# Kernel tuning notes

Hardware: AMD Instinct MI355X
Metric: run time of the kernel (lower is better)

The kernel has to match this reference:

```python
import jax, jax.numpy as jnp
import numpy as np

SIGMA = 0.5          # cone height of the distance field
B, NV, NF, MAXC = 32, 6890, 13776, 8
NC = NF * MAXC       # padded number of collision pair slots


def setup_inputs() -> dict:
    key = jax.random.key(0)
    ks = jax.random.split(key, 8)
    return {
        "pose": jax.random.normal(ks[0], (B, 72), jnp.float32),
        "joints": jax.random.normal(ks[1], (B, 24, 3), jnp.float32),
        "points": jax.random.normal(ks[2], (B, 118, 3), jnp.float32),
        "keypoints": jax.random.normal(ks[3], (B, 118, 3), jnp.float32),
        "vertices": jax.random.normal(ks[4], (B, NV, 3), jnp.float32),
        "weight": jnp.ones((1,), jnp.float32),
        "faces": jax.random.randint(ks[5], (NF, 3), 0, NV, dtype=jnp.int32),
        "collision_idxs": jax.random.randint(ks[6], (B, NC, 2), 0, NF, dtype=jnp.int32),
    }


def _cone_point2plane(cone_tris, query_tris):
    """Conic distance-field penetration (point2plane), vectorized over pairs.
    cone_tris/query_tris: [B, C, 3 verts, 3 xyz]. Returns [B, C]."""
    c = cone_tris.mean(axis=-2)                              # centroid [B,C,3]
    e1 = cone_tris[..., 1, :] - cone_tris[..., 0, :]
    e2 = cone_tris[..., 2, :] - cone_tris[..., 0, :]
    n = jnp.cross(e1, e2)
    n = n / (jnp.linalg.norm(n, axis=-1, keepdims=True) + 1e-8)
    d = query_tris - c[..., None, :]                         # [B,C,3,3]
    h = jnp.einsum('bcvk,bck->bcv', d, n)                    # signed plane dist
    r = jnp.linalg.norm(d, axis=-1)                          # dist to centroid
    phi = jnp.maximum(SIGMA - r, 0.0)                        # linear cone field
    pen = jnp.where(h < 0, phi * h * h, 0.0)                 # penetrating verts only
    return pen.sum(axis=-1)


def reference(pose, joints, points, keypoints, vertices, weight, faces, collision_idxs):
    # polygons = verts.view(-1,3)[faces_idx]  ->  per-batch face gather
    tris = jnp.take(vertices, faces, axis=1)                 # [B,NF,3,3]
    recv_idx = collision_idxs[..., 0]
    intr_idx = collision_idxs[..., 1]
    valid = recv_idx >= 0                                    # -1 padding slots

    def gather(idx):
        idx = jnp.maximum(idx, 0)[:, :, None, None]
        return jnp.take_along_axis(tris, idx, axis=1)        # [B,NC,3,3]

    recv = gather(recv_idx)
    intr = gather(intr_idx)
    # symmetric penetration: intruder verts in receiver's field and vice versa
    pen = _cone_point2plane(recv, intr) + _cone_point2plane(intr, recv)
    loss = jnp.where(valid, pen, 0.0).sum() / B
    return loss * weight[0]
```

## Files before the change

### kernel.cpp

```cpp
#include <hip/hip_runtime.h>

#define SIGMA 0.5f
#define BB 32
#define NVV 6890
#define NFF 13776
#define MAXC 8
#define NCC (NFF * MAXC)

#define SLOTS 8
#define PAIRS_PER_SLOT (NCC / SLOTS)
#define QHALF (PAIRS_PER_SLOT / 4)
#define THREADS 1024
#define NBLOCK (BB * SLOTS)

typedef int       v4i __attribute__((ext_vector_type(4)));
typedef _Float16  h4  __attribute__((ext_vector_type(4)));

__device__ __forceinline__ float3 loadv3(const float* __restrict__ p) {
    return make_float3(p[0], p[1], p[2]);
}

__device__ __forceinline__ float fsqrt(float x) { return __builtin_amdgcn_sqrtf(x); }
__device__ __forceinline__ float frcp(float x)  { return __builtin_amdgcn_rcpf(x); }

__device__ __forceinline__ float coneSide(float cx, float cy, float cz,
                                          float nx, float ny, float nz,
                                          float3 q0, float3 q1, float3 q2) {
    float pen = 0.0f;
#pragma unroll
    for (int v = 0; v < 3; ++v) {
        float3 q = (v == 0) ? q0 : ((v == 1) ? q1 : q2);
        float dx = q.x - cx, dy = q.y - cy, dz = q.z - cz;
        float h  = dx * nx + dy * ny + dz * nz;
        float r2 = dx * dx + dy * dy + dz * dz;
        float r  = fsqrt(r2);
        float phi = fmaxf(SIGMA - r, 0.0f);
        float hm  = fminf(h, 0.0f);
        pen = fmaf(phi * hm, hm, pen);
    }
    return pen;
}

__device__ __forceinline__ float triPairPen(float3 A0, float3 A1, float3 A2,
                                            float3 B0, float3 B1, float3 B2) {
    const float third = 1.0f / 3.0f;
    float cax = (A0.x + A1.x + A2.x) * third;
    float cay = (A0.y + A1.y + A2.y) * third;
    float caz = (A0.z + A1.z + A2.z) * third;
    float cbx = (B0.x + B1.x + B2.x) * third;
    float cby = (B0.y + B1.y + B2.y) * third;
    float cbz = (B0.z + B1.z + B2.z) * third;
    float e1x = A1.x - A0.x, e1y = A1.y - A0.y, e1z = A1.z - A0.z;
    float e2x = A2.x - A0.x, e2y = A2.y - A0.y, e2z = A2.z - A0.z;
    float nax = e1y * e2z - e1z * e2y;
    float nay = e1z * e2x - e1x * e2z;
    float naz = e1x * e2y - e1y * e2x;
    float inva = frcp(fsqrt(nax * nax + nay * nay + naz * naz) + 1e-8f);
    nax *= inva; nay *= inva; naz *= inva;
    float f1x = B1.x - B0.x, f1y = B1.y - B0.y, f1z = B1.z - B0.z;
    float f2x = B2.x - B0.x, f2y = B2.y - B0.y, f2z = B2.z - B0.z;
    float nbx = f1y * f2z - f1z * f2y;
    float nby = f1z * f2x - f1x * f2z;
    float nbz = f1x * f2y - f1y * f2x;
    float invb = frcp(fsqrt(nbx * nbx + nby * nby + nbz * nbz) + 1e-8f);
    nbx *= invb; nby *= invb; nbz *= invb;

    return coneSide(cax, cay, caz, nax, nay, naz, B0, B1, B2)
         + coneSide(cbx, cby, cbz, nbx, nby, nbz, A0, A1, A2);
}

__device__ __forceinline__ float3 ldsVertB(const h4* __restrict__ sv, unsigned int boff) {
    h4 h = *(const h4*)((const char*)sv + boff);
    return make_float3((float)h.x, (float)h.y, (float)h.z);
}

__device__ __forceinline__ float pairPen(const h4* __restrict__ sv,
                                         const unsigned int*   __restrict__ f01,
                                         const unsigned short* __restrict__ f2,
                                         int r, int it) {
    const int rr = r  < 0 ? 0 : r;
    const int g  = it < 0 ? 0 : it;
    unsigned int wa  = f01[rr];
    unsigned int wb  = f01[g];
    unsigned int oa2 = f2[rr];
    unsigned int ob2 = f2[g];
    float3 A0 = ldsVertB(sv, wa & 0xFFFFu);
    float3 A1 = ldsVertB(sv, wa >> 16);
    float3 A2 = ldsVertB(sv, oa2);
    float3 B0 = ldsVertB(sv, wb & 0xFFFFu);
    float3 B1 = ldsVertB(sv, wb >> 16);
    float3 B2 = ldsVertB(sv, ob2);
    float pen = triPairPen(A0, A1, A2, B0, B1, B2);
    return r < 0 ? 0.0f : pen;
}

__global__ __launch_bounds__(THREADS) void fused_kernel(
    const float* __restrict__ vertices,
    const int*   __restrict__ faces,
    const int*   __restrict__ cidx,
    float*       __restrict__ partials)
{
    __shared__ h4             s_v[NVV];
    __shared__ unsigned int   s_f01[NFF];
    __shared__ unsigned short s_f2[NFF];
    __shared__ float          s_red[16];

    const int b   = blockIdx.x;
    const int sl  = blockIdx.y;
    const int tid = threadIdx.x;

    const float* vb = vertices + (size_t)b * (NVV * 3);
    for (int v = tid; v < NVV; v += THREADS) {
        const float* p = vb + 3 * v;
        h4 h;
        h.x = (_Float16)p[0];
        h.y = (_Float16)p[1];
        h.z = (_Float16)p[2];
        h.w = (_Float16)0.0f;
        s_v[v] = h;
    }

    for (int f = tid; f < NFF; f += THREADS) {
        int i0 = faces[3 * f + 0];
        int i1 = faces[3 * f + 1];
        int i2 = faces[3 * f + 2];
        s_f01[f] = (unsigned int)(i0 << 3) | ((unsigned int)(i1 << 3) << 16);
        s_f2[f]  = (unsigned short)(i2 << 3);
    }
    __syncthreads();

    float pen = 0.0f;
    const v4i* c4 = (const v4i*)(cidx + ((size_t)b * NCC + (size_t)sl * PAIRS_PER_SLOT) * 2);
    for (int q = tid; q < QHALF; q += THREADS) {
        v4i pA = __builtin_nontemporal_load(c4 + q);
        v4i pB = __builtin_nontemporal_load(c4 + q + QHALF);
        float p0 = pairPen(s_v, s_f01, s_f2, pA.x, pA.y);
        float p1 = pairPen(s_v, s_f01, s_f2, pA.z, pA.w);
        float p2 = pairPen(s_v, s_f01, s_f2, pB.x, pB.y);
        float p3 = pairPen(s_v, s_f01, s_f2, pB.z, pB.w);
        pen += (p0 + p1) + (p2 + p3);
    }

#pragma unroll
    for (int off = 32; off > 0; off >>= 1)
        pen += __shfl_down(pen, off, 64);
    const int lane = tid & 63;
    const int wv   = tid >> 6;
    if (lane == 0) s_red[wv] = pen;
    __syncthreads();
    if (tid == 0) {
        float t = 0.0f;
#pragma unroll
        for (int w = 0; w < 16; ++w) t += s_red[w];
        partials[b * SLOTS + sl] = t;
    }
}

__global__ __launch_bounds__(256) void fin2_kernel(
    const float* __restrict__ partials,
    const float* __restrict__ weight,
    float*       __restrict__ out)
{
    float s = partials[threadIdx.x];
#pragma unroll
    for (int off = 32; off > 0; off >>= 1)
        s += __shfl_down(s, off, 64);
    __shared__ float smem[4];
    const int lane = threadIdx.x & 63;
    const int wv   = threadIdx.x >> 6;
    if (lane == 0) smem[wv] = s;
    __syncthreads();
    if (threadIdx.x == 0)
        out[0] = (smem[0] + smem[1] + smem[2] + smem[3]) * weight[0] * (1.0f / (float)BB);
}

__global__ void init_kernel(float* __restrict__ accum) { accum[0] = 0.0f; }

__global__ __launch_bounds__(256) void pen_direct(
    const float* __restrict__ vertices, const int* __restrict__ faces,
    const int2* __restrict__ cidx, float* __restrict__ accum)
{
    const int i = blockIdx.x * blockDim.x + threadIdx.x;
    float pen = 0.0f;
    if (i < BB * NCC) {
        const int b = i / NCC;
        const int2 pr = cidx[i];
        if (pr.x >= 0) {
            const int f0 = pr.x;
            const int f1 = pr.y < 0 ? 0 : pr.y;
            const float* vb = vertices + (size_t)b * (NVV * 3);
            float3 a0 = loadv3(vb + (size_t)faces[f0*3+0] * 3);
            float3 a1 = loadv3(vb + (size_t)faces[f0*3+1] * 3);
            float3 a2 = loadv3(vb + (size_t)faces[f0*3+2] * 3);
            float3 b0 = loadv3(vb + (size_t)faces[f1*3+0] * 3);
            float3 b1 = loadv3(vb + (size_t)faces[f1*3+1] * 3);
            float3 b2 = loadv3(vb + (size_t)faces[f1*3+2] * 3);
            pen = triPairPen(a0, a1, a2, b0, b1, b2);
        }
    }
#pragma unroll
    for (int off = 32; off > 0; off >>= 1)
        pen += __shfl_down(pen, off, 64);
    __shared__ float smem[4];
    const int lane = threadIdx.x & 63;
    const int wv   = threadIdx.x >> 6;
    if (lane == 0) smem[wv] = pen;
    __syncthreads();
    if (threadIdx.x == 0)
        atomicAdd(accum, smem[0] + smem[1] + smem[2] + smem[3]);
}

__global__ void fin_kernel(const float* __restrict__ accum,
                           const float* __restrict__ weight,
                           float* __restrict__ out)
{
    out[0] = accum[0] * weight[0] * (1.0f / (float)BB);
}

extern "C" void kernel_launch(void* const* d_in, const int* in_sizes, int n_in,
                              void* d_out, int out_size, void* d_ws, size_t ws_size,
                              hipStream_t stream) {
    const float* vertices = (const float*)d_in[4];
    const float* weight   = (const float*)d_in[5];
    const int*   faces    = (const int*)d_in[6];
    const int*   cidx     = (const int*)d_in[7];
    float* out = (float*)d_out;

    if (ws_size >= NBLOCK * sizeof(float)) {
        float* partials = (float*)d_ws;
        fused_kernel<<<dim3(BB, SLOTS), dim3(THREADS), 0, stream>>>(
            vertices, faces, cidx, partials);
        fin2_kernel<<<dim3(1), dim3(256), 0, stream>>>(partials, weight, out);
    } else {
        float* accum = (float*)d_ws;
        const int totalPairs = BB * NCC;
        init_kernel<<<dim3(1), dim3(1), 0, stream>>>(accum);
        pen_direct<<<dim3((totalPairs + 255) / 256), dim3(256), 0, stream>>>(
            vertices, faces, (const int2*)cidx, accum);
        fin_kernel<<<dim3(1), dim3(1), 0, stream>>>(accum, weight, out);
    }
}
```

Measured before the change: 111.8 us.

## Move packed face table to global memory and double slot count

Face index packing moves out of the main kernel into a separate pack kernel that writes a uint2 table to workspace. The fused kernel then reads face offsets from global (L2-cached) memory instead of rebuilding them in LDS for every block. This removes a redundant per-block face pass and shrinks LDS to just the fp16 vertex cache, so more blocks can fit per CU. Slots go from 8 to 16, which doubles the grid to 512 blocks. The cost is that every vertex lookup now follows a global-memory gather, and vertices are still re-staged into LDS by twice as many blocks.

Measured after the change: 135.6 us. 21.3% more time.

```diff
diff --git a/kernel.cpp b/kernel.cpp
--- a/kernel.cpp
+++ b/kernel.cpp
@@ -7,11 +7,14 @@
 #define MAXC 8
 #define NCC (NFF * MAXC)
 
-#define SLOTS 8
+#define SLOTS 16
 #define PAIRS_PER_SLOT (NCC / SLOTS)
-#define QHALF (PAIRS_PER_SLOT / 4)
+#define QUADS (PAIRS_PER_SLOT / 2)
 #define THREADS 1024
 #define NBLOCK (BB * SLOTS)
+
+#define FTAB_BYTES ((size_t)NFF * 8)
+#define WS_NEED (FTAB_BYTES + (size_t)NBLOCK * 4 + 64)
 
 typedef int       v4i __attribute__((ext_vector_type(4)));
 typedef _Float16  h4  __attribute__((ext_vector_type(4)));
@@ -74,36 +77,43 @@
     return make_float3((float)h.x, (float)h.y, (float)h.z);
 }
 
-__device__ __forceinline__ float pairPen(const h4* __restrict__ sv,
-                                         const unsigned int*   __restrict__ f01,
-                                         const unsigned short* __restrict__ f2,
+__device__ __forceinline__ float pairPen(const h4*   __restrict__ sv,
+                                         const uint2* __restrict__ ftab,
                                          int r, int it) {
     const int rr = r  < 0 ? 0 : r;
     const int g  = it < 0 ? 0 : it;
-    unsigned int wa  = f01[rr];
-    unsigned int wb  = f01[g];
-    unsigned int oa2 = f2[rr];
-    unsigned int ob2 = f2[g];
-    float3 A0 = ldsVertB(sv, wa & 0xFFFFu);
-    float3 A1 = ldsVertB(sv, wa >> 16);
-    float3 A2 = ldsVertB(sv, oa2);
-    float3 B0 = ldsVertB(sv, wb & 0xFFFFu);
-    float3 B1 = ldsVertB(sv, wb >> 16);
-    float3 B2 = ldsVertB(sv, ob2);
+    uint2 fa = ftab[rr];
+    uint2 fb = ftab[g];
+    float3 A0 = ldsVertB(sv, fa.x & 0xFFFFu);
+    float3 A1 = ldsVertB(sv, fa.x >> 16);
+    float3 A2 = ldsVertB(sv, fa.y);
+    float3 B0 = ldsVertB(sv, fb.x & 0xFFFFu);
+    float3 B1 = ldsVertB(sv, fb.x >> 16);
+    float3 B2 = ldsVertB(sv, fb.y);
     float pen = triPairPen(A0, A1, A2, B0, B1, B2);
     return r < 0 ? 0.0f : pen;
 }
 
-__global__ __launch_bounds__(THREADS) void fused_kernel(
+__global__ __launch_bounds__(256) void pack_kernel(
+    const int* __restrict__ faces,
+    uint2*     __restrict__ ftab)
+{
+    const int f = blockIdx.x * 256 + threadIdx.x;
+    if (f >= NFF) return;
+    const unsigned int o0 = (unsigned int)(faces[3 * f + 0] << 3);
+    const unsigned int o1 = (unsigned int)(faces[3 * f + 1] << 3);
+    const unsigned int o2 = (unsigned int)(faces[3 * f + 2] << 3);
+    ftab[f] = make_uint2(o0 | (o1 << 16), o2);
+}
+
+__global__ __launch_bounds__(THREADS, 8) void fused_kernel(
     const float* __restrict__ vertices,
-    const int*   __restrict__ faces,
+    const uint2* __restrict__ ftab,
     const int*   __restrict__ cidx,
     float*       __restrict__ partials)
 {
-    __shared__ h4             s_v[NVV];
-    __shared__ unsigned int   s_f01[NFF];
-    __shared__ unsigned short s_f2[NFF];
-    __shared__ float          s_red[16];
+    __shared__ h4    s_v[NVV];
+    __shared__ float s_red[16];
 
     const int b   = blockIdx.x;
     const int sl  = blockIdx.y;
@@ -119,26 +129,15 @@
         h.w = (_Float16)0.0f;
         s_v[v] = h;
     }
-
-    for (int f = tid; f < NFF; f += THREADS) {
-        int i0 = faces[3 * f + 0];
-        int i1 = faces[3 * f + 1];
-        int i2 = faces[3 * f + 2];
-        s_f01[f] = (unsigned int)(i0 << 3) | ((unsigned int)(i1 << 3) << 16);
-        s_f2[f]  = (unsigned short)(i2 << 3);
-    }
     __syncthreads();
 
     float pen = 0.0f;
     const v4i* c4 = (const v4i*)(cidx + ((size_t)b * NCC + (size_t)sl * PAIRS_PER_SLOT) * 2);
-    for (int q = tid; q < QHALF; q += THREADS) {
-        v4i pA = __builtin_nontemporal_load(c4 + q);
-        v4i pB = __builtin_nontemporal_load(c4 + q + QHALF);
-        float p0 = pairPen(s_v, s_f01, s_f2, pA.x, pA.y);
-        float p1 = pairPen(s_v, s_f01, s_f2, pA.z, pA.w);
-        float p2 = pairPen(s_v, s_f01, s_f2, pB.x, pB.y);
-        float p3 = pairPen(s_v, s_f01, s_f2, pB.z, pB.w);
-        pen += (p0 + p1) + (p2 + p3);
+    for (int q = tid; q < QUADS; q += THREADS) {
+        v4i pr = __builtin_nontemporal_load(c4 + q);
+        float p0 = pairPen(s_v, ftab, pr.x, pr.y);
+        float p1 = pairPen(s_v, ftab, pr.z, pr.w);
+        pen += p0 + p1;
     }
 
 #pragma unroll
@@ -156,7 +155,7 @@
     }
 }
 
-__global__ __launch_bounds__(256) void fin2_kernel(
+__global__ __launch_bounds__(512) void fin2_kernel(
     const float* __restrict__ partials,
     const float* __restrict__ weight,
     float*       __restrict__ out)
@@ -165,13 +164,17 @@
 #pragma unroll
     for (int off = 32; off > 0; off >>= 1)
         s += __shfl_down(s, off, 64);
-    __shared__ float smem[4];
+    __shared__ float smem[8];
     const int lane = threadIdx.x & 63;
     const int wv   = threadIdx.x >> 6;
     if (lane == 0) smem[wv] = s;
     __syncthreads();
-    if (threadIdx.x == 0)
-        out[0] = (smem[0] + smem[1] + smem[2] + smem[3]) * weight[0] * (1.0f / (float)BB);
+    if (threadIdx.x == 0) {
+        float t = 0.0f;
+#pragma unroll
+        for (int w = 0; w < 8; ++w) t += smem[w];
+        out[0] = t * weight[0] * (1.0f / (float)BB);
+    }
 }
 
 __global__ void init_kernel(float* __restrict__ accum) { accum[0] = 0.0f; }
@@ -226,11 +229,14 @@
     const int*   cidx     = (const int*)d_in[7];
     float* out = (float*)d_out;
 
-    if (ws_size >= NBLOCK * sizeof(float)) {
-        float* partials = (float*)d_ws;
+    if (ws_size >= WS_NEED) {
+        uint2* ftab     = (uint2*)d_ws;
+        float* partials = (float*)((char*)d_ws + FTAB_BYTES);
+
+        pack_kernel<<<dim3((NFF + 255) / 256), dim3(256), 0, stream>>>(faces, ftab);
         fused_kernel<<<dim3(BB, SLOTS), dim3(THREADS), 0, stream>>>(
-            vertices, faces, cidx, partials);
-        fin2_kernel<<<dim3(1), dim3(256), 0, stream>>>(partials, weight, out);
+            vertices, ftab, cidx, partials);
+        fin2_kernel<<<dim3(1), dim3(512), 0, stream>>>(partials, weight, out);
     } else {
         float* accum = (float*)d_ws;
         const int totalPairs = BB * NCC;
```
